# Kernel tuning notes

Measured on AMD Instinct MI355X. Metric: run time of the kernel, lower is better.

The kernel has to match this reference:

```python
import jax, jax.numpy as jnp
import numpy as np

B, N, D = 16, 2048, 1024


def _linear_params(key, d, scale):
    kw, kb = jax.random.split(key)
    W = jax.random.uniform(kw, (d, d), jnp.float32, -scale, scale)
    b = jax.random.uniform(kb, (d,), jnp.float32, -scale, scale)
    return W, b


def setup_inputs() -> dict:
    key = jax.random.key(0)
    ks = jax.random.split(key, 9)
    scale = 1.0 / np.sqrt(D)  # torch nn.Linear default init range
    x1 = jax.random.normal(ks[0], (B, N, D), jnp.float32)
    x2 = jax.random.normal(ks[1], (B, N, D), jnp.float32)
    Wq, bq = _linear_params(ks[2], D, scale)
    Wk, bk = _linear_params(ks[3], D, scale)
    Wv, bv = _linear_params(ks[4], D, scale)
    W1, b1 = _linear_params(ks[5], D, scale)
    W2, b2 = _linear_params(ks[6], D, scale)
    W3, b3 = _linear_params(ks[7], D, scale)
    # torch init is zeros(1); use small nonzero so output/grad paths are exercised
    gamma = jax.random.normal(ks[8], (1,), jnp.float32) * 0.1
    return {"x1": x1, "x2": x2, "Wq": Wq, "bq": bq, "Wk": Wk, "bk": bk,
            "Wv": Wv, "bv": bv, "W1": W1, "b1": b1, "W2": W2, "b2": b2,
            "W3": W3, "b3": b3, "gamma": gamma}


def reference(x1, x2, Wq, bq, Wk, bk, Wv, bv, W1, b1, W2, b2, W3, b3, gamma):
    # QKV cross-attention (unscaled softmax, as in the torch source)
    q = jnp.einsum('bnd,ed->bne', x1, Wq) + bq
    k = jnp.einsum('bnd,ed->bne', x2, Wk) + bk
    v = jnp.einsum('bnd,ed->bne', x2, Wv) + bv
    energy = jnp.einsum('bik,bjk->bij', q, k)          # [B, N, N]
    attn = jax.nn.softmax(energy, axis=-1)
    out = jnp.einsum('bij,bjk->bik', attn, v)          # [B, N, D]
    # multiscale sigmoid gate: sigmoid(s1 + s2 + s3)
    s = (jnp.einsum('bnd,ed->bne', out, W1) + b1
         + jnp.einsum('bnd,ed->bne', out, W2) + b2
         + jnp.einsum('bnd,ed->bne', out, W3) + b3)
    out = out * jax.nn.sigmoid(s)
    return gamma * out + x1
```

## Files before the change

### kernel.cpp

```cpp
#include <hip/hip_runtime.h>
#include <hip/hip_bf16.h>
#include <hip/hip_fp16.h>
#include <cstdint>

#define B_ 16
#define N_ 2048
#define D_ 1024

typedef __attribute__((ext_vector_type(4))) float f32x4;
typedef __attribute__((ext_vector_type(8))) short s16x8;

typedef __attribute__((address_space(1))) const void* gas_ptr;
typedef __attribute__((address_space(3))) void* las_ptr;

__device__ __forceinline__ void gload16(const void* g, void* l)
{
    __builtin_amdgcn_global_load_lds((gas_ptr)(uintptr_t)g, (las_ptr)(uintptr_t)l, 16, 0, 0);
}

__device__ __forceinline__ ushort f2bf(float f)
{
    union { __hip_bfloat16 h; ushort u; } c;
    c.h = __float2bfloat16(f);
    return c.u;
}
__device__ __forceinline__ float bf2f(ushort u)
{
    union { __hip_bfloat16 h; ushort u; } c;
    c.u = u;
    return __bfloat162float(c.h);
}

__global__ __launch_bounds__(256)
void cvt_bf16(const float* __restrict__ in, ushort* __restrict__ out, long n)
{
    long i = ((long)blockIdx.x * 256 + threadIdx.x) * 8;
    const long stride = (long)gridDim.x * 256 * 8;
    for (; i < n; i += stride) {
        f32x4 a = *(const f32x4*)(in + i);
        f32x4 b = *(const f32x4*)(in + i + 4);
        s16x8 o;
#pragma unroll
        for (int j = 0; j < 4; ++j) { o[j] = (short)f2bf(a[j]); o[4 + j] = (short)f2bf(b[j]); }
        *(s16x8*)(out + i) = o;
    }
}

__global__ __launch_bounds__(256)
void prep_w(const float* __restrict__ Wq, const float* __restrict__ Wk, const float* __restrict__ Wv,
            const float* __restrict__ W1, const float* __restrict__ W2, const float* __restrict__ W3,
            const float* __restrict__ b1, const float* __restrict__ b2, const float* __restrict__ b3,
            ushort* __restrict__ wq, ushort* __restrict__ wk, ushort* __restrict__ wv,
            ushort* __restrict__ wsum, float* __restrict__ bsum)
{
    const long i = ((long)blockIdx.x * 256 + threadIdx.x) * 4;
    if (i < (long)D_ * D_) {
#pragma unroll
        for (int j = 0; j < 4; ++j) {
            wq[i + j] = f2bf(Wq[i + j]);
            wk[i + j] = f2bf(Wk[i + j]);
            wv[i + j] = f2bf(Wv[i + j]);
            wsum[i + j] = f2bf(W1[i + j] + W2[i + j] + W3[i + j]);
        }
        if (i < D_) {
#pragma unroll
            for (int j = 0; j < 4; ++j) bsum[i + j] = b1[i + j] + b2[i + j] + b3[i + j];
        }
    }
}

template<int EPI>
__global__ __launch_bounds__(512, 2)
void gemm256(const ushort* __restrict__ A, const ushort* __restrict__ Bw,
             void* __restrict__ Out, const float* __restrict__ bias,
             int Nn, int K, int NT,
             long sA, long sB, long sO,
             const ushort* __restrict__ outb, const float* __restrict__ x1r,
             const float* __restrict__ gamma)
{
    __shared__ ushort lds[65536];
    const int tid = threadIdx.x;
    const int l = tid & 63;
    const int w = tid >> 6;
    const int wm = w >> 2, wn = w & 3;
    const int lr = l & 15;
    const int c2x = ((((l >> 4) * 16) ^ ((lr & 8) << 2)) >> 1);

    const int gx = gridDim.x, gy = gridDim.y;
    const int nwg = gx * gy * (int)gridDim.z;
    const int orig = ((int)blockIdx.z * gy + blockIdx.y) * gx + blockIdx.x;
    const int swzb = (orig & 7) * (nwg >> 3) + (orig >> 3);
    const int gxy = gx * gy;
    const int bz = swzb / gxy;
    const int rem = swzb - bz * gxy;
    const int by = rem / gx;
    const int bx = rem - by * gx;
    const int m0 = by * 256, n0 = bx * 256;

    const ushort* Ab = A + (long)bz * sA;
    const ushort* Bb = Bw + (long)bz * sB;

    int srow[2], scol[2];
#pragma unroll
    for (int i = 0; i < 2; ++i) {
        const int L = (i * 512 + tid) * 16;
        const int P = L ^ (((L >> 9) & 1) << 5);
        srow[i] = (P >> 6) & 127;
        scol[i] = ((P >> 13) << 5) | ((P & 63) >> 1);
    }
    const int sdst = w * 512;

    f32x4 acc[8][4];
#pragma unroll
    for (int i = 0; i < 8; ++i)
#pragma unroll
        for (int j = 0; j < 4; ++j) acc[i][j] = f32x4{0.f, 0.f, 0.f, 0.f};
    s16x8 a[4][2], b[2][2][2];

#define STAGEH(pl, t)                                                                     \
    if ((t) < NT) {                                                                       \
        const int rb2 = (t) & 1;                                                          \
        const long kk = (long)(t) << 6;                                                   \
        _Pragma("unroll")                                                                 \
        for (int i = 0; i < 2; ++i) {                                                     \
            if ((pl) < 2)                                                                 \
                gload16(Ab + (long)(m0 + (pl) * 128 + srow[i]) * K + kk + scol[i],        \
                        &lds[rb2 * 16384 + (pl) * 8192 + sdst + i * 4096]);               \
            else                                                                          \
                gload16(Bb + (long)(n0 + ((pl) - 2) * 128 + srow[i]) * K + kk + scol[i],  \
                        &lds[32768 + rb2 * 16384 + ((pl) - 2) * 8192 + sdst + i * 4096]); \
        }                                                                                 \
    }

#define LDA_(qm)                                                                           \
    _Pragma("unroll") for (int mi = 0; mi < 4; ++mi)                                       \
    _Pragma("unroll") for (int ks = 0; ks < 2; ++ks)                                       \
        a[mi][ks] = *(const s16x8*)&lds[rbase_a + ks * 4096 + ((qm) * 64 + mi * 16 + lr) * 32 + c2x];

#define LDB_(qn)                                                                           \
    _Pragma("unroll") for (int ni = 0; ni < 2; ++ni)                                       \
    _Pragma("unroll") for (int ks = 0; ks < 2; ++ks)                                       \
        b[qn][ni][ks] = *(const s16x8*)&lds[rbase_b + ks * 4096 +                          \
            ((wn & 1) * 64 + (qn) * 32 + ni * 16 + lr) * 32 + c2x];

#define MM_(qm, qn)                                                                        \
    __builtin_amdgcn_s_setprio(1);                                                         \
    _Pragma("unroll") for (int mi = 0; mi < 4; ++mi)                                       \
    _Pragma("unroll") for (int ni = 0; ni < 2; ++ni)                                       \
    _Pragma("unroll") for (int ks = 0; ks < 2; ++ks)                                       \
        acc[(qm) * 4 + mi][(qn) * 2 + ni] = __builtin_amdgcn_mfma_f32_16x16x32_bf16(       \
            a[mi][ks], b[qn][ni][ks], acc[(qm) * 4 + mi][(qn) * 2 + ni], 0, 0, 0);         \
    __builtin_amdgcn_s_setprio(0);

#define BARR __builtin_amdgcn_s_barrier()
#define LGKM0 do { asm volatile("s_waitcnt lgkmcnt(0)" ::: "memory"); \
                   __builtin_amdgcn_sched_barrier(0); } while (0)

#define KGROUP(tt, VMSTR) {                                          \
    const int rb = (tt) & 1;                                         \
    const int rbase_a = rb * 16384 + wm * 8192;                      \
    const int rbase_b = 32768 + rb * 16384 + (wn >> 1) * 8192;       \
                                                            \
    LDB_(0); LDA_(0);                                                \
    BARR; LGKM0; MM_(0, 0); BARR;                                    \
                                 \
    LDB_(1);                                                         \
    BARR; LGKM0; MM_(0, 1); BARR;                                    \
               \
    LDA_(1);                                                         \
    STAGEH(2, (tt) + 2);                                             \
    STAGEH(3, (tt) + 2);                                             \
    BARR; LGKM0; MM_(1, 0); BARR;                                    \
               \
    MM_(1, 1);                                                       \
    STAGEH(0, (tt) + 2);                                             \
    STAGEH(1, (tt) + 2);                                             \
    asm volatile("s_waitcnt " VMSTR ::: "memory");                   \
    BARR; }

    STAGEH(0, 0); STAGEH(1, 0); STAGEH(2, 0); STAGEH(3, 0);
    STAGEH(0, 1); STAGEH(1, 1); STAGEH(2, 1); STAGEH(3, 1);
    asm volatile("s_waitcnt vmcnt(8)" ::: "memory");
    BARR;

    int t = 0;
    for (; t < NT - 2; ++t) KGROUP(t, "vmcnt(8)");
    for (; t < NT; ++t) KGROUP(t, "vmcnt(0)");

#undef KGROUP
#undef STAGEH
#undef LDA_
#undef LDB_
#undef MM_

    float gam = 0.f;
    if (EPI == 3) gam = *gamma;
#pragma unroll
    for (int am = 0; am < 8; ++am) {
#pragma unroll
        for (int an = 0; an < 4; ++an) {
#pragma unroll
            for (int r = 0; r < 4; ++r) {
                const int m = m0 + wm * 128 + am * 16 + (l >> 4) * 4 + r;
                const int n = n0 + wn * 64 + an * 16 + lr;
                const float v = acc[am][an][r];
                const long o = (long)bz * sO + (long)m * Nn + n;
                if (EPI == 0) {
                    ((ushort*)Out)[o] = f2bf(v + bias[n]);
                } else if (EPI == 1) {
                    union { __half h; ushort u; } c;
                    c.h = __float2half(v);
                    ((ushort*)Out)[o] = c.u;
                } else if (EPI == 2) {
                    ((ushort*)Out)[o] = f2bf(v);
                } else if (EPI == 4) {
                    ((ushort*)Out)[o] = f2bf(v + bias[m]);
                } else {
                    const float s = v + bias[n];
                    const float g = 1.f / (1.f + __expf(-s));
                    const float ov = bf2f(outb[(long)m * Nn + n]);
                    ((float*)Out)[o] = gam * ov * g + x1r[(long)m * Nn + n];
                }
            }
        }
    }
}

__global__ __launch_bounds__(256)
void softmax_inplace(ushort* __restrict__ EA)
{
    const long row = blockIdx.x;
    ushort* p = EA + row * N_;
    const int tid = threadIdx.x;
    const int c0 = tid * 8;
    __shared__ float red[8];

    s16x8 raw = *(const s16x8*)(p + c0);
    float v[8];
    float mx = -3.0e38f;
#pragma unroll
    for (int i = 0; i < 8; ++i) {
        union { ushort u; __half h; } c;
        c.u = (ushort)raw[i];
        v[i] = __half2float(c.h);
        mx = fmaxf(mx, v[i]);
    }
#pragma unroll
    for (int off = 32; off > 0; off >>= 1) mx = fmaxf(mx, __shfl_xor(mx, off));
    if ((tid & 63) == 0) red[tid >> 6] = mx;
    __syncthreads();
    mx = fmaxf(fmaxf(red[0], red[1]), fmaxf(red[2], red[3]));

    float s = 0.f;
#pragma unroll
    for (int i = 0; i < 8; ++i) { v[i] = __expf(v[i] - mx); s += v[i]; }
#pragma unroll
    for (int off = 32; off > 0; off >>= 1) s += __shfl_xor(s, off);
    if ((tid & 63) == 0) red[4 + (tid >> 6)] = s;
    __syncthreads();
    s = (red[4] + red[5]) + (red[6] + red[7]);
    const float inv = 1.f / s;

    s16x8 o;
#pragma unroll
    for (int i = 0; i < 8; ++i) o[i] = (short)f2bf(v[i] * inv);
    *(s16x8*)(p + c0) = o;
}

extern "C" void kernel_launch(void* const* d_in, const int* in_sizes, int n_in,
                              void* d_out, int out_size, void* d_ws, size_t ws_size,
                              hipStream_t stream)
{
    const float* x1 = (const float*)d_in[0];
    const float* x2 = (const float*)d_in[1];
    const float* Wq = (const float*)d_in[2];
    const float* bq = (const float*)d_in[3];
    const float* Wk = (const float*)d_in[4];
    const float* bk = (const float*)d_in[5];
    const float* Wv = (const float*)d_in[6];
    const float* bv = (const float*)d_in[7];
    const float* W1 = (const float*)d_in[8];
    const float* b1 = (const float*)d_in[9];
    const float* W2 = (const float*)d_in[10];
    const float* b2 = (const float*)d_in[11];
    const float* W3 = (const float*)d_in[12];
    const float* b3 = (const float*)d_in[13];
    const float* gamma = (const float*)d_in[14];
    float* out = (float*)d_out;

    char* ws = (char*)d_ws;
    const long SZ_XB = (long)B_ * N_ * D_ * 2;
    ushort* x1b  = (ushort*)(ws);
    ushort* x2b  = (ushort*)(ws + SZ_XB);
    ushort* EA   = (ushort*)(ws);
    ushort* wqb  = (ushort*)(ws + 2 * SZ_XB);
    ushort* wkb  = (ushort*)(ws + 2 * SZ_XB + 1L * 2097152);
    ushort* wvb  = (ushort*)(ws + 2 * SZ_XB + 2L * 2097152);
    ushort* wsb  = (ushort*)(ws + 2 * SZ_XB + 3L * 2097152);
    float*  bsum = (float*) (ws + 2 * SZ_XB + 4L * 2097152);
    char* base2  = ws + 2 * SZ_XB + 4L * 2097152 + 4096;
    ushort* Qb   = (ushort*)(base2);
    ushort* Kb   = (ushort*)(base2 + SZ_XB);
    ushort* Vtb  = (ushort*)(base2 + 2 * SZ_XB);
    ushort* outb = Kb;

    const long NE = (long)B_ * N_ * D_;

    cvt_bf16<<<4096, 256, 0, stream>>>(x1, x1b, NE);
    cvt_bf16<<<4096, 256, 0, stream>>>(x2, x2b, NE);
    prep_w<<<1024, 256, 0, stream>>>(Wq, Wk, Wv, W1, W2, W3, b1, b2, b3,
                                     wqb, wkb, wvb, wsb, bsum);

    gemm256<0><<<dim3(4, 128, 1), 512, 0, stream>>>(x1b, wqb, Qb, bq,
        D_, D_, 16, 0, 0, 0, nullptr, nullptr, nullptr);
    gemm256<0><<<dim3(4, 128, 1), 512, 0, stream>>>(x2b, wkb, Kb, bk,
        D_, D_, 16, 0, 0, 0, nullptr, nullptr, nullptr);

    gemm256<4><<<dim3(8, 4, 16), 512, 0, stream>>>(wvb, x2b, Vtb, bv,
        N_, D_, 16, 0, (long)N_ * D_, (long)D_ * N_,
        nullptr, nullptr, nullptr);

    gemm256<1><<<dim3(8, 8, 16), 512, 0, stream>>>(Qb, Kb, EA, nullptr,
        N_, D_, 16, (long)N_ * D_, (long)N_ * D_, (long)N_ * N_,
        nullptr, nullptr, nullptr);

    softmax_inplace<<<B_ * N_, 256, 0, stream>>>(EA);

    gemm256<2><<<dim3(4, 8, 16), 512, 0, stream>>>(EA, Vtb, outb, nullptr,
        D_, N_, 32, (long)N_ * N_, (long)D_ * N_, (long)N_ * D_,
        nullptr, nullptr, nullptr);

    gemm256<3><<<dim3(4, 128, 1), 512, 0, stream>>>(outb, wsb, out, bsum,
        D_, D_, 16, 0, 0, 0, outb, x1, gamma);
}
```

Baseline: 739.0 us.

## Switch GEMM main loop to single-stage prefetch with fewer barriers

Reworks the GEMM K-loop pipeline so that all four global-to-LDS staging loads for the next tile are issued at the start of each iteration, with a prefetch distance of one instead of two. The per-quadrant workgroup barriers are dropped, leaving one barrier per iteration after waiting for all vector-memory loads. The goal is to cut barrier and synchronisation overhead between MFMA phases. In exchange there is less prefetch depth to hide global-memory latency, and a full vmcnt(0) wait every iteration. Staging into the other LDS buffer while the current one is being read relies on double buffering still being correct with the shorter distance.

After: 754.4 us. +2.1%, slower.

```diff
diff --git a/kernel.cpp b/kernel.cpp
--- a/kernel.cpp
+++ b/kernel.cpp
@@ -153,39 +153,34 @@
     __builtin_amdgcn_s_setprio(0);
 
 #define BARR __builtin_amdgcn_s_barrier()
-#define LGKM0 do { asm volatile("s_waitcnt lgkmcnt(0)" ::: "memory"); \
-                   __builtin_amdgcn_sched_barrier(0); } while (0)
-
-#define KGROUP(tt, VMSTR) {                                          \
+#define S0 __builtin_amdgcn_sched_barrier(0)
+#define LGKM0 do { asm volatile("s_waitcnt lgkmcnt(0)" ::: "memory"); S0; } while (0)
+
+#define KGROUP(tt) {                                                 \
     const int rb = (tt) & 1;                                         \
     const int rbase_a = rb * 16384 + wm * 8192;                      \
     const int rbase_b = 32768 + rb * 16384 + (wn >> 1) * 8192;       \
-                                                            \
+      \
     LDB_(0); LDA_(0);                                                \
-    BARR; LGKM0; MM_(0, 0); BARR;                                    \
-                                 \
-    LDB_(1);                                                         \
-    BARR; LGKM0; MM_(0, 1); BARR;                                    \
-               \
-    LDA_(1);                                                         \
-    STAGEH(2, (tt) + 2);                                             \
-    STAGEH(3, (tt) + 2);                                             \
-    BARR; LGKM0; MM_(1, 0); BARR;                                    \
-               \
+    STAGEH(0, (tt) + 1); STAGEH(1, (tt) + 1);                        \
+    STAGEH(2, (tt) + 1); STAGEH(3, (tt) + 1);                        \
+    LGKM0;                                                           \
+    LDB_(1); S0;                                                     \
+    MM_(0, 0);                                                       \
+    LGKM0;                                                           \
+    MM_(0, 1);                                                       \
+    LDA_(1); S0;                                                     \
+    LGKM0;                                                           \
+    MM_(1, 0);                                                       \
     MM_(1, 1);                                                       \
-    STAGEH(0, (tt) + 2);                                             \
-    STAGEH(1, (tt) + 2);                                             \
-    asm volatile("s_waitcnt " VMSTR ::: "memory");                   \
+    asm volatile("s_waitcnt vmcnt(0)" ::: "memory"); S0;             \
     BARR; }
 
     STAGEH(0, 0); STAGEH(1, 0); STAGEH(2, 0); STAGEH(3, 0);
-    STAGEH(0, 1); STAGEH(1, 1); STAGEH(2, 1); STAGEH(3, 1);
-    asm volatile("s_waitcnt vmcnt(8)" ::: "memory");
+    asm volatile("s_waitcnt vmcnt(0)" ::: "memory");
     BARR;
 
-    int t = 0;
-    for (; t < NT - 2; ++t) KGROUP(t, "vmcnt(8)");
-    for (; t < NT; ++t) KGROUP(t, "vmcnt(0)");
+    for (int t = 0; t < NT; ++t) KGROUP(t);
 
 #undef KGROUP
 #undef STAGEH
```

## Switch GEMM to 32x32x16 MFMA and finer-grained load staging

Applied to the files above, without the earlier changes.

Replaces the 16x16x32 bf16 MFMA tiles with 32x32x16 MFMA instructions, reworking the LDS read addressing, the accumulator layout and the epilogue index mapping to match. The larger MFMA needs fewer LDS fragment reads per FLOP and fewer instructions. The global-to-LDS prefetch schedule is also reorganised: quarter-tiles for step t+1 are issued interleaved within the current k-group rather than prefetching two steps ahead, and the vmcnt waits are tightened. This changes the prefetch distance, which could expose memory latency, and the new swizzled addressing carries a risk of bank conflicts or layout mistakes.

Measured after the change: 766.0 us. 3.7% more time.

```diff
diff --git a/kernel.cpp b/kernel.cpp
--- a/kernel.cpp
+++ b/kernel.cpp
@@ -8,6 +8,7 @@
 #define D_ 1024
 
 typedef __attribute__((ext_vector_type(4))) float f32x4;
+typedef __attribute__((ext_vector_type(16))) float f32x16;
 typedef __attribute__((ext_vector_type(8))) short s16x8;
 
 typedef __attribute__((address_space(1))) const void* gas_ptr;
@@ -83,8 +84,8 @@
     const int l = tid & 63;
     const int w = tid >> 6;
     const int wm = w >> 2, wn = w & 3;
-    const int lr = l & 15;
-    const int c2x = ((((l >> 4) * 16) ^ ((lr & 8) << 2)) >> 1);
+    const int rA = l & 31;
+    const int slotbase = (((l >> 3) & 1) << 1) | ((l >> 5) & 1);
 
     const int gx = gridDim.x, gy = gridDim.y;
     const int nwg = gx * gy * (int)gridDim.z;
@@ -110,12 +111,14 @@
     }
     const int sdst = w * 512;
 
-    f32x4 acc[8][4];
-#pragma unroll
-    for (int i = 0; i < 8; ++i)
-#pragma unroll
-        for (int j = 0; j < 4; ++j) acc[i][j] = f32x4{0.f, 0.f, 0.f, 0.f};
-    s16x8 a[4][2], b[2][2][2];
+    f32x16 acc[4][2];
+#pragma unroll
+    for (int i = 0; i < 4; ++i)
+#pragma unroll
+        for (int j = 0; j < 2; ++j)
+#pragma unroll
+            for (int r = 0; r < 16; ++r) acc[i][j][r] = 0.f;
+    s16x8 a[2][4], b[2][4];
 
 #define STAGEH(pl, t)                                                                     \
     if ((t) < NT) {                                                                       \
@@ -132,24 +135,23 @@
         }                                                                                 \
     }
 
-#define LDA_(qm)                                                                           \
-    _Pragma("unroll") for (int mi = 0; mi < 4; ++mi)                                       \
-    _Pragma("unroll") for (int ks = 0; ks < 2; ++ks)                                       \
-        a[mi][ks] = *(const s16x8*)&lds[rbase_a + ks * 4096 + ((qm) * 64 + mi * 16 + lr) * 32 + c2x];
-
-#define LDB_(qn)                                                                           \
-    _Pragma("unroll") for (int ni = 0; ni < 2; ++ni)                                       \
-    _Pragma("unroll") for (int ks = 0; ks < 2; ++ks)                                       \
-        b[qn][ni][ks] = *(const s16x8*)&lds[rbase_b + ks * 4096 +                          \
-            ((wn & 1) * 64 + (qn) * 32 + ni * 16 + lr) * 32 + c2x];
-
-#define MM_(qm, qn)                                                                        \
+#define LDA_(h)                                                                            \
+    _Pragma("unroll") for (int f2 = 0; f2 < 2; ++f2)                                       \
+    _Pragma("unroll") for (int ks = 0; ks < 4; ++ks)                                       \
+        a[f2][ks] = *(const s16x8*)&lds[rbase_a + (ks >> 1) * 4096 +                       \
+            (((h) * 2 + f2) * 32 + rA) * 32 + ((slotbase ^ ((ks & 1) << 1)) << 3)];
+
+#define LDB_(c)                                                                            \
+    _Pragma("unroll") for (int ks = 0; ks < 4; ++ks)                                       \
+        b[c][ks] = *(const s16x8*)&lds[rbase_b + (ks >> 1) * 4096 +                        \
+            ((wn & 1) * 64 + (c) * 32 + rA) * 32 + ((slotbase ^ ((ks & 1) << 1)) << 3)];
+
+#define MM_(h, c)                                                                          \
     __builtin_amdgcn_s_setprio(1);                                                         \
-    _Pragma("unroll") for (int mi = 0; mi < 4; ++mi)                                       \
-    _Pragma("unroll") for (int ni = 0; ni < 2; ++ni)                                       \
-    _Pragma("unroll") for (int ks = 0; ks < 2; ++ks)                                       \
-        acc[(qm) * 4 + mi][(qn) * 2 + ni] = __builtin_amdgcn_mfma_f32_16x16x32_bf16(       \
-            a[mi][ks], b[qn][ni][ks], acc[(qm) * 4 + mi][(qn) * 2 + ni], 0, 0, 0);         \
+    _Pragma("unroll") for (int f2 = 0; f2 < 2; ++f2)                                       \
+    _Pragma("unroll") for (int ks = 0; ks < 4; ++ks)                                       \
+        acc[(h) * 2 + f2][c] = __builtin_amdgcn_mfma_f32_32x32x16_bf16(                    \
+            a[f2][ks], b[c][ks], acc[(h) * 2 + f2][c], 0, 0, 0);                           \
     __builtin_amdgcn_s_setprio(0);
 
 #define BARR __builtin_amdgcn_s_barrier()
@@ -162,29 +164,29 @@
     const int rbase_b = 32768 + rb * 16384 + (wn >> 1) * 8192;       \
                                                             \
     LDB_(0); LDA_(0);                                                \
+    STAGEH(1, (tt) + 1);                                             \
     BARR; LGKM0; MM_(0, 0); BARR;                                    \
-                                 \
+                                                            \
     LDB_(1);                                                         \
+    STAGEH(2, (tt) + 1);                                             \
     BARR; LGKM0; MM_(0, 1); BARR;                                    \
-               \
+                                                            \
     LDA_(1);                                                         \
-    STAGEH(2, (tt) + 2);                                             \
-    STAGEH(3, (tt) + 2);                                             \
+    STAGEH(3, (tt) + 1);                                             \
     BARR; LGKM0; MM_(1, 0); BARR;                                    \
-               \
+     \
     MM_(1, 1);                                                       \
     STAGEH(0, (tt) + 2);                                             \
-    STAGEH(1, (tt) + 2);                                             \
     asm volatile("s_waitcnt " VMSTR ::: "memory");                   \
     BARR; }
 
     STAGEH(0, 0); STAGEH(1, 0); STAGEH(2, 0); STAGEH(3, 0);
-    STAGEH(0, 1); STAGEH(1, 1); STAGEH(2, 1); STAGEH(3, 1);
-    asm volatile("s_waitcnt vmcnt(8)" ::: "memory");
+    STAGEH(0, 1);
+    asm volatile("s_waitcnt vmcnt(2)" ::: "memory");
     BARR;
 
     int t = 0;
-    for (; t < NT - 2; ++t) KGROUP(t, "vmcnt(8)");
+    for (; t < NT - 2; ++t) KGROUP(t, "vmcnt(2)");
     for (; t < NT; ++t) KGROUP(t, "vmcnt(0)");
 
 #undef KGROUP
@@ -195,15 +197,17 @@
 
     float gam = 0.f;
     if (EPI == 3) gam = *gamma;
-#pragma unroll
-    for (int am = 0; am < 8; ++am) {
-#pragma unroll
-        for (int an = 0; an < 4; ++an) {
-#pragma unroll
-            for (int r = 0; r < 4; ++r) {
-                const int m = m0 + wm * 128 + am * 16 + (l >> 4) * 4 + r;
-                const int n = n0 + wn * 64 + an * 16 + lr;
-                const float v = acc[am][an][r];
+    const int rowoff = (l >> 5) << 2;
+    const int ncol = l & 31;
+#pragma unroll
+    for (int af = 0; af < 4; ++af) {
+#pragma unroll
+        for (int bf = 0; bf < 2; ++bf) {
+#pragma unroll
+            for (int r = 0; r < 16; ++r) {
+                const int m = m0 + wm * 128 + af * 32 + (r & 3) + ((r >> 2) << 3) + rowoff;
+                const int n = n0 + wn * 64 + bf * 32 + ncol;
+                const float v = acc[af][bf][r];
                 const long o = (long)bz * sO + (long)m * Nn + n;
                 if (EPI == 0) {
                     ((ushort*)Out)[o] = f2bf(v + bias[n]);
```
